# Performance work log

Measured on AMD Instinct MI355X. Metric: run time of the kernel, lower is better.

The kernel has to match this reference:

```python
import jax, jax.numpy as jnp
import numpy as np

B, N, C, L = 32, 1024, 128, 4

def setup_inputs() -> dict:
    key = jax.random.key(0)
    ks = jax.random.split(key, 8)
    x = jax.random.normal(ks[0], (B, N, C), dtype=jnp.float32)
    # binary adjacency: nonzero entries become unit-weight edges (edge weights unused in module)
    adj = jax.random.randint(ks[1], (B, N, N), 0, 2).astype(jnp.float32)
    mask = jnp.ones((B, N), dtype=jnp.float32)
    s = 1.0 / np.sqrt(C)
    weight = jax.random.uniform(ks[2], (L, C, C), minval=-s, maxval=s, dtype=jnp.float32)
    w_ih = jax.random.uniform(ks[3], (L, 3 * C, C), minval=-s, maxval=s, dtype=jnp.float32)
    w_hh = jax.random.uniform(ks[4], (L, 3 * C, C), minval=-s, maxval=s, dtype=jnp.float32)
    b_ih = jax.random.uniform(ks[5], (L, 3 * C), minval=-s, maxval=s, dtype=jnp.float32)
    b_hh = jax.random.uniform(ks[6], (L, 3 * C), minval=-s, maxval=s, dtype=jnp.float32)
    return {"x": x, "adj": adj, "mask": mask, "weight": weight,
            "w_ih": w_ih, "w_hh": w_hh, "b_ih": b_ih, "b_hh": b_hh}

def _gru_cell(m, h, w_ih, w_hh, b_ih, b_hh):
    # PyTorch GRUCell, gate order (r, z, n)
    gx = m @ w_ih.T + b_ih
    gh = h @ w_hh.T + b_hh
    xr, xz, xn = jnp.split(gx, 3, axis=-1)
    hr, hz, hn = jnp.split(gh, 3, axis=-1)
    r = jax.nn.sigmoid(xr + hr)
    z = jax.nn.sigmoid(xz + hz)
    n = jnp.tanh(xn + r * hn)
    return (1.0 - z) * n + z * h

def reference(x, adj, mask, weight, w_ih, w_hh, b_ih, b_hh):
    h = x  # [B, N, C]; in_channels == out_channels so no zero-padding needed
    for i in range(L):
        hw = jnp.einsum('bnc,cd->bnd', h, weight[i])
        # scatter-add of messages source->target == A^T @ (h W), unit edge weights
        m = jnp.einsum('bjn,bjd->bnd', adj, hw)
        h = _gru_cell(m, h, w_ih[i], w_hh[i], b_ih[i], b_hh[i])
    return h * mask[:, :, None]
```

## Files before the change

### kernel.cpp

```cpp
#include <hip/hip_runtime.h>
#include <stdint.h>


#define NB 32
#define NN 1024
#define NC 128
#define NL 4
#define MTOT (NB * NN)

#define MP 136

typedef __attribute__((ext_vector_type(8))) short s16x8;
typedef __attribute__((ext_vector_type(4))) float f32x4;
typedef __attribute__((ext_vector_type(2))) unsigned int u32x2;
typedef unsigned short U16;
typedef unsigned int U32;

__device__ __forceinline__ U16 f2bf(float f) {
    union { float f; U32 u; } v; v.f = f;
    return (U16)((v.u + 0x7FFFu + ((v.u >> 16) & 1u)) >> 16);
}
__device__ __forceinline__ float bf2f(U16 h) {
    union { U32 u; float f; } v; v.u = ((U32)h) << 16;
    return v.f;
}
__device__ __forceinline__ void splitbf(float x, U16& hi, U16& lo) {
    hi = f2bf(x);
    lo = f2bf(x - bf2f(hi));
}
__device__ __forceinline__ float sigmoidf_(float x) { return 1.f / (1.f + __expf(-x)); }

__device__ __forceinline__ void glds16(const void* g, void* l) {
    __builtin_amdgcn_global_load_lds(
        (const __attribute__((address_space(1))) void*)g,
        (__attribute__((address_space(3))) void*)l, 16, 0, 0);
}

#define SWZ(row, g) ((row) * 64 + ((((g) ^ ((row) & 7))) * 8))

__global__ __launch_bounds__(256) void k_setup(
    const float* __restrict__ adj, U16* __restrict__ adjT,
    const float* __restrict__ w, const float* __restrict__ wih, const float* __restrict__ whh,
    U16* __restrict__ wThi, U16* __restrict__ wTlo,
    U16* __restrict__ wihhi, U16* __restrict__ wihlo,
    U16* __restrict__ whhhi, U16* __restrict__ whhlo,
    const float* __restrict__ x, U16* __restrict__ hhi, U16* __restrict__ hlo)
{
    __shared__ float t[64 * 65];
    const int bid = blockIdx.x, tid = threadIdx.x;
    if (bid < 8192) {
        const int b = bid >> 8, rem = bid & 255;
        const int j0 = (rem & 15) * 64, n0 = (rem >> 4) * 64;
        const int rr = tid >> 4, c4 = (tid & 15) * 4;
#pragma unroll
        for (int p = 0; p < 4; ++p) {
            int j = p * 16 + rr;
            f32x4 v = *(const f32x4*)&adj[((size_t)b << 20) + ((size_t)(j0 + j) << 10) + n0 + c4];
#pragma unroll
            for (int u = 0; u < 4; ++u) t[j * 65 + c4 + u] = v[u];
        }
        __syncthreads();
#pragma unroll
        for (int p = 0; p < 4; ++p) {
            int n = p * 16 + rr;
            U16 h0 = f2bf(t[(c4 + 0) * 65 + n]);
            U16 h1 = f2bf(t[(c4 + 1) * 65 + n]);
            U16 h2 = f2bf(t[(c4 + 2) * 65 + n]);
            U16 h3 = f2bf(t[(c4 + 3) * 65 + n]);
            u32x2 pk; pk[0] = (U32)h0 | ((U32)h1 << 16); pk[1] = (U32)h2 | ((U32)h3 << 16);
            *(u32x2*)&adjT[((size_t)b << 20) + ((size_t)(n0 + n) << 10) + j0 + c4] = pk;
        }
    } else if (bid < 9984) {
        int i = (bid - 8192) * 256 + tid;
        if (i < 65536) {
            int l = i >> 14, rem = i & 16383, c = rem >> 7, d = rem & 127;
            U16 hi, lo; splitbf(w[i], hi, lo);
            int o = (l << 14) + (d << 7) + c;
            wThi[o] = hi; wTlo[o] = lo;
        } else if (i < 262144) {
            int j = i - 65536;
            U16 hi, lo; splitbf(wih[j], hi, lo);
            wihhi[j] = hi; wihlo[j] = lo;
        } else {
            int j = i - 262144;
            U16 hi, lo; splitbf(whh[j], hi, lo);
            whhhi[j] = hi; whhlo[j] = lo;
        }
    } else {
        int base = (bid - 9984) * 2048 + tid;
#pragma unroll
        for (int p = 0; p < 8; ++p) {
            int i = base + p * 256;
            U16 hi, lo; splitbf(x[i], hi, lo);
            hhi[i] = hi; hlo[i] = lo;
        }
    }
}

__global__ __launch_bounds__(256, 4) void k_hw2(
    const U16* __restrict__ Ahi, const U16* __restrict__ Alo,
    const U16* __restrict__ Bhi, const U16* __restrict__ Blo,
    U16* __restrict__ Ohi, U16* __restrict__ Olo)
{
    __shared__ union {
        struct { U16 Bh[128 * 64]; U16 Bl[128 * 64]; } bs;
        float bounce[64 * 129];
    } u;
    const int tid = threadIdx.x;
    const int lane = tid & 63, wv = tid >> 6;
    const int wd0 = wv * 32;
    const int lm = lane & 15, lk8 = (lane >> 4) * 8, quad = lane >> 4;
    const int m0 = blockIdx.x * 64;

    f32x4 acc[4][2] = {};

    for (int kc = 0; kc < 128; kc += 64) {
#pragma unroll
        for (int t = 0; t < 4; ++t) {
            int li = tid + t * 256; int d = li >> 3, sg = li & 7;
            int go = d * 128 + kc + ((sg ^ (d & 7)) * 8);
            glds16(&Bhi[go], &u.bs.Bh[li * 8]);
            glds16(&Blo[go], &u.bs.Bl[li * 8]);
        }
        __syncthreads();
#pragma unroll
        for (int ks = 0; ks < 2; ++ks) {
            const int k0 = kc + ks * 32 + lk8;
            const int g = ks * 4 + quad;
            s16x8 ahi[4], alo[4], bhi[2], blo[2];
#pragma unroll
            for (int q = 0; q < 4; ++q) {
                size_t ao = (size_t)(m0 + q * 16 + lm) * 128 + k0;
                ahi[q] = *(const s16x8*)&Ahi[ao];
                alo[q] = *(const s16x8*)&Alo[ao];
            }
#pragma unroll
            for (int q = 0; q < 2; ++q) {
                bhi[q] = *(const s16x8*)&u.bs.Bh[SWZ(wd0 + q * 16 + lm, g)];
                blo[q] = *(const s16x8*)&u.bs.Bl[SWZ(wd0 + q * 16 + lm, g)];
            }
#pragma unroll
            for (int rt = 0; rt < 4; ++rt)
#pragma unroll
                for (int ct = 0; ct < 2; ++ct) {
                    f32x4 a = acc[rt][ct];
                    a = __builtin_amdgcn_mfma_f32_16x16x32_bf16(ahi[rt], bhi[ct], a, 0, 0, 0);
                    a = __builtin_amdgcn_mfma_f32_16x16x32_bf16(ahi[rt], blo[ct], a, 0, 0, 0);
                    a = __builtin_amdgcn_mfma_f32_16x16x32_bf16(alo[rt], bhi[ct], a, 0, 0, 0);
                    acc[rt][ct] = a;
                }
        }
        __syncthreads();
    }

#pragma unroll
    for (int rt = 0; rt < 4; ++rt)
#pragma unroll
        for (int ct = 0; ct < 2; ++ct)
#pragma unroll
            for (int r = 0; r < 4; ++r)
                u.bounce[(rt * 16 + quad * 4 + r) * 129 + wd0 + ct * 16 + lm] = acc[rt][ct][r];
    __syncthreads();
    const int b = m0 >> 10, j0 = m0 & 1023;
#pragma unroll
    for (int t = 0; t < 16; ++t) {
        int i = tid + t * 256; int d = i >> 5, j2 = (i & 31) * 2;
        float x0 = u.bounce[j2 * 129 + d], x1 = u.bounce[(j2 + 1) * 129 + d];
        U16 h0, l0, h1, l1; splitbf(x0, h0, l0); splitbf(x1, h1, l1);
        size_t o = (((size_t)(b * 128 + d)) << 10) + j0 + j2;
        *(U32*)&Ohi[o] = (U32)h0 | ((U32)h1 << 16);
        *(U32*)&Olo[o] = (U32)l0 | ((U32)l1 << 16);
    }
}

__global__ __launch_bounds__(256, 2) void k_mega6(
    const U16* __restrict__ adjT,
    const U16* __restrict__ hwThi, const U16* __restrict__ hwTlo,
    const U16* __restrict__ hhi, const U16* __restrict__ hlo,
    const U16* __restrict__ wihhi, const U16* __restrict__ wihlo,
    const U16* __restrict__ whhhi, const U16* __restrict__ whhlo,
    const float* __restrict__ bih, const float* __restrict__ bhh,
    const float* __restrict__ mask,
    U16* __restrict__ houthi, U16* __restrict__ houtlo,
    float* __restrict__ out, int last)
{
    __shared__ union {
        struct { U16 As[2][64 * 64]; U16 Bh[2][128 * 64]; U16 Bl[2][128 * 64]; } st;
        struct { U16 Mhi[64 * MP]; U16 Mlo[64 * MP]; } m;
    } u;
    const int tid = threadIdx.x;
    const int lane = tid & 63, wv = tid >> 6;
    const int wd0 = wv * 32;
    const int lm = lane & 15, lk8 = (lane >> 4) * 8, quad = lane >> 4;
    const int xcd = blockIdx.x & 7;
    const int j = blockIdx.x >> 3;
    const int bt = xcd * 4 + (j >> 4);
    const int n0 = (j & 15) * 64;
    const int row0 = bt * NN + n0;

#define STAGE(kc, b)                                                                     \
    {                                                                                    \
        _Pragma("unroll")                                                                \
        for (int t = 0; t < 2; ++t) {                                                    \
            int li = tid + t * 256; int r = li >> 3, sg = li & 7;                        \
            glds16(&adjT[((size_t)bt << 20) + ((size_t)(n0 + r) << 10) + (kc)            \
                         + ((sg ^ (r & 7)) * 8)],                                        \
                   &u.st.As[b][li * 8]);                                                 \
        }                                                                                \
        _Pragma("unroll")                                                                \
        for (int t = 0; t < 4; ++t) {                                                    \
            int li = tid + t * 256; int d = li >> 3, sg = li & 7;                        \
            size_t o = (((size_t)(bt * 128 + d)) << 10) + (kc) + ((sg ^ (d & 7)) * 8);   \
            glds16(&hwThi[o], &u.st.Bh[b][li * 8]);                                      \
            glds16(&hwTlo[o], &u.st.Bl[b][li * 8]);                                      \
        }                                                                                \
    }

    f32x4 macc[4][2] = {};
    STAGE(0, 0);
    for (int c = 0; c < 16; ++c) {
        const int b = c & 1;
        __syncthreads();
        if (c + 1 < 16) STAGE((c + 1) * 64, b ^ 1);
#pragma unroll
        for (int ks = 0; ks < 2; ++ks) {
            const int g = ks * 4 + quad;
            s16x8 a[4], bh[2], bl[2];
#pragma unroll
            for (int q = 0; q < 4; ++q)
                a[q] = *(const s16x8*)&u.st.As[b][SWZ(q * 16 + lm, g)];
#pragma unroll
            for (int q = 0; q < 2; ++q) {
                bh[q] = *(const s16x8*)&u.st.Bh[b][SWZ(wd0 + q * 16 + lm, g)];
                bl[q] = *(const s16x8*)&u.st.Bl[b][SWZ(wd0 + q * 16 + lm, g)];
            }
#pragma unroll
            for (int rt = 0; rt < 4; ++rt)
#pragma unroll
                for (int ct = 0; ct < 2; ++ct) {
                    f32x4 cc = macc[rt][ct];
                    cc = __builtin_amdgcn_mfma_f32_16x16x32_bf16(a[rt], bh[ct], cc, 0, 0, 0);
                    cc = __builtin_amdgcn_mfma_f32_16x16x32_bf16(a[rt], bl[ct], cc, 0, 0, 0);
                    macc[rt][ct] = cc;
                }
        }
    }
#undef STAGE
    __syncthreads();

#pragma unroll
    for (int rt = 0; rt < 4; ++rt)
#pragma unroll
        for (int ct = 0; ct < 2; ++ct)
#pragma unroll
            for (int rr = 0; rr < 4; ++rr) {
                int rloc = rt * 16 + quad * 4 + rr;
                int d = wd0 + ct * 16 + lm;
                U16 hi, lo; splitbf(macc[rt][ct][rr], hi, lo);
                u.m.Mhi[rloc * MP + d] = hi;
                u.m.Mlo[rloc * MP + d] = lo;
            }

    f32x4 aR[4][2], aZ[4][2], aXN[4][2], aHN[4][2];
#pragma unroll
    for (int ct = 0; ct < 2; ++ct) {
        const int col = wd0 + ct * 16 + lm;
        const float bR  = bih[col]       + bhh[col];
        const float bZ  = bih[128 + col] + bhh[128 + col];
        const float bXN = bih[256 + col];
        const float bHN = bhh[256 + col];
#pragma unroll
        for (int rt = 0; rt < 4; ++rt) {
            aR[rt][ct]  = f32x4{bR, bR, bR, bR};
            aZ[rt][ct]  = f32x4{bZ, bZ, bZ, bZ};
            aXN[rt][ct] = f32x4{bXN, bXN, bXN, bXN};
            aHN[rt][ct] = f32x4{bHN, bHN, bHN, bHN};
        }
    }

    for (int cc = 0; cc < 4; ++cc) {
        const int ch = (cc + 2) & 3;
        if (cc == 2) __syncthreads();
        const U16* __restrict__ Whi = (ch < 2) ? wihhi : whhhi;
        const U16* __restrict__ Wlo = (ch < 2) ? wihlo : whhlo;
        const int kb = (ch & 1) * 64;
#pragma unroll
        for (int ks = 0; ks < 2; ++ks) {
            const int ko = kb + ks * 32 + lk8;
            s16x8 ahi[4], alo[4];
            if (ch < 2) {
#pragma unroll
                for (int q = 0; q < 4; ++q) {
                    ahi[q] = *(const s16x8*)&u.m.Mhi[(q * 16 + lm) * MP + ko];
                    alo[q] = *(const s16x8*)&u.m.Mlo[(q * 16 + lm) * MP + ko];
                }
            } else {
#pragma unroll
                for (int q = 0; q < 4; ++q) {
                    size_t ao = (size_t)(row0 + q * 16 + lm) * 128 + ko;
                    ahi[q] = *(const s16x8*)&hhi[ao];
                    alo[q] = *(const s16x8*)&hlo[ao];
                }
            }
#pragma unroll
            for (int ct = 0; ct < 2; ++ct) {
                const int col = wd0 + ct * 16 + lm;
                s16x8 bhiR = *(const s16x8*)&Whi[(size_t)col * 128 + ko];
                s16x8 bloR = *(const s16x8*)&Wlo[(size_t)col * 128 + ko];
                s16x8 bhiZ = *(const s16x8*)&Whi[(size_t)(128 + col) * 128 + ko];
                s16x8 bloZ = *(const s16x8*)&Wlo[(size_t)(128 + col) * 128 + ko];
                s16x8 bhiN = *(const s16x8*)&Whi[(size_t)(256 + col) * 128 + ko];
                s16x8 bloN = *(const s16x8*)&Wlo[(size_t)(256 + col) * 128 + ko];
#pragma unroll
                for (int rt = 0; rt < 4; ++rt) {
                    f32x4 r = aR[rt][ct];
                    r = __builtin_amdgcn_mfma_f32_16x16x32_bf16(ahi[rt], bhiR, r, 0, 0, 0);
                    r = __builtin_amdgcn_mfma_f32_16x16x32_bf16(ahi[rt], bloR, r, 0, 0, 0);
                    r = __builtin_amdgcn_mfma_f32_16x16x32_bf16(alo[rt], bhiR, r, 0, 0, 0);
                    aR[rt][ct] = r;
                    f32x4 z = aZ[rt][ct];
                    z = __builtin_amdgcn_mfma_f32_16x16x32_bf16(ahi[rt], bhiZ, z, 0, 0, 0);
                    z = __builtin_amdgcn_mfma_f32_16x16x32_bf16(ahi[rt], bloZ, z, 0, 0, 0);
                    z = __builtin_amdgcn_mfma_f32_16x16x32_bf16(alo[rt], bhiZ, z, 0, 0, 0);
                    aZ[rt][ct] = z;
                }
                if (ch < 2) {
#pragma unroll
                    for (int rt = 0; rt < 4; ++rt) {
                        f32x4 n = aXN[rt][ct];
                        n = __builtin_amdgcn_mfma_f32_16x16x32_bf16(ahi[rt], bhiN, n, 0, 0, 0);
                        n = __builtin_amdgcn_mfma_f32_16x16x32_bf16(ahi[rt], bloN, n, 0, 0, 0);
                        n = __builtin_amdgcn_mfma_f32_16x16x32_bf16(alo[rt], bhiN, n, 0, 0, 0);
                        aXN[rt][ct] = n;
                    }
                } else {
#pragma unroll
                    for (int rt = 0; rt < 4; ++rt) {
                        f32x4 n = aHN[rt][ct];
                        n = __builtin_amdgcn_mfma_f32_16x16x32_bf16(ahi[rt], bhiN, n, 0, 0, 0);
                        n = __builtin_amdgcn_mfma_f32_16x16x32_bf16(ahi[rt], bloN, n, 0, 0, 0);
                        n = __builtin_amdgcn_mfma_f32_16x16x32_bf16(alo[rt], bhiN, n, 0, 0, 0);
                        aHN[rt][ct] = n;
                    }
                }
            }
        }
    }

#pragma unroll
    for (int rt = 0; rt < 4; ++rt) {
#pragma unroll
        for (int ct = 0; ct < 2; ++ct) {
            const int col = wd0 + ct * 16 + lm;
#pragma unroll
            for (int rr = 0; rr < 4; ++rr) {
                const int row = row0 + rt * 16 + quad * 4 + rr;
                float r = sigmoidf_(aR[rt][ct][rr]);
                float z = sigmoidf_(aZ[rt][ct][rr]);
                float n = tanhf(aXN[rt][ct][rr] + r * aHN[rt][ct][rr]);
                size_t ho = (size_t)row * 128 + col;
                float hv = bf2f(hhi[ho]) + bf2f(hlo[ho]);
                float hnew = (1.f - z) * n + z * hv;
                if (last) {
                    out[ho] = hnew * mask[row];
                } else {
                    U16 hi2, lo2; splitbf(hnew, hi2, lo2);
                    houthi[ho] = hi2;
                    houtlo[ho] = lo2;
                }
            }
        }
    }
}

extern "C" void kernel_launch(void* const* d_in, const int* in_sizes, int n_in,
                              void* d_out, int out_size, void* d_ws, size_t ws_size,
                              hipStream_t stream) {
    (void)in_sizes; (void)n_in; (void)out_size; (void)ws_size;
    const float* x    = (const float*)d_in[0];
    const float* adj  = (const float*)d_in[1];
    const float* mask = (const float*)d_in[2];
    const float* wgt  = (const float*)d_in[3];
    const float* wih  = (const float*)d_in[4];
    const float* whh  = (const float*)d_in[5];
    const float* bih  = (const float*)d_in[6];
    const float* bhh  = (const float*)d_in[7];
    float* out = (float*)d_out;

    char* p = (char*)d_ws;
    U16* adjT    = (U16*)p;                p += (size_t)NB * NN * NN * 2;
    U16* h_hi    = (U16*)p;                p += (size_t)MTOT * NC * 2;
    U16* h_lo    = (U16*)p;                p += (size_t)MTOT * NC * 2;
    U16* hwT_hi  = (U16*)p;                p += (size_t)NB * NC * NN * 2;
    U16* hwT_lo  = (U16*)p;                p += (size_t)NB * NC * NN * 2;
    U16* wT_hi   = (U16*)p;                p += (size_t)NL * NC * NC * 2;
    U16* wT_lo   = (U16*)p;                p += (size_t)NL * NC * NC * 2;
    U16* wih_hi  = (U16*)p;                p += (size_t)NL * 384 * NC * 2;
    U16* wih_lo  = (U16*)p;                p += (size_t)NL * 384 * NC * 2;
    U16* whh_hi  = (U16*)p;                p += (size_t)NL * 384 * NC * 2;
    U16* whh_lo  = (U16*)p;                p += (size_t)NL * 384 * NC * 2;

    k_setup<<<12032, 256, 0, stream>>>(adj, adjT, wgt, wih, whh,
                                       wT_hi, wT_lo, wih_hi, wih_lo, whh_hi, whh_lo,
                                       x, h_hi, h_lo);

    for (int l = 0; l < NL; ++l) {
        k_hw2<<<512, 256, 0, stream>>>(h_hi, h_lo,
                                       wT_hi + l * 16384, wT_lo + l * 16384,
                                       hwT_hi, hwT_lo);
        k_mega6<<<512, 256, 0, stream>>>(adjT, hwT_hi, hwT_lo, h_hi, h_lo,
                                         wih_hi + l * 49152, wih_lo + l * 49152,
                                         whh_hi + l * 49152, whh_lo + l * 49152,
                                         bih + l * 384, bhh + l * 384, mask,
                                         h_hi, h_lo, out, (l == NL - 1) ? 1 : 0);
    }
}
```

Measured before the change: 519.7 us.

## Reassociate to (A^T h) W and fuse weight GEMM into mega kernel

Drops the separate h·W kernel by computing the aggregation A^T·h first and then multiplying by W inside the fused GRU kernel, using associativity. Each layer writes a transposed hi/lo copy of the new hidden state through an LDS bounce buffer, ping-ponged between two buffers, and setup produces the initial transposed x. This removes one launch per layer and the global write/read of hwT. In exchange the mega kernel does an extra in-LDS GEMM with weights read from global, and the rounding of the intermediate product changes.

```diff
diff --git a/kernel.cpp b/kernel.cpp
--- a/kernel.cpp
+++ b/kernel.cpp
@@ -44,7 +44,8 @@
     U16* __restrict__ wThi, U16* __restrict__ wTlo,
     U16* __restrict__ wihhi, U16* __restrict__ wihlo,
     U16* __restrict__ whhhi, U16* __restrict__ whhlo,
-    const float* __restrict__ x, U16* __restrict__ hhi, U16* __restrict__ hlo)
+    const float* __restrict__ x, U16* __restrict__ hhi, U16* __restrict__ hlo,
+    U16* __restrict__ hThi, U16* __restrict__ hTlo)
 {
     __shared__ float t[64 * 65];
     const int bid = blockIdx.x, tid = threadIdx.x;
@@ -70,8 +71,35 @@
             u32x2 pk; pk[0] = (U32)h0 | ((U32)h1 << 16); pk[1] = (U32)h2 | ((U32)h3 << 16);
             *(u32x2*)&adjT[((size_t)b << 20) + ((size_t)(n0 + n) << 10) + j0 + c4] = pk;
         }
-    } else if (bid < 9984) {
-        int i = (bid - 8192) * 256 + tid;
+    } else if (bid < 9216) {
+        const int bid2 = bid - 8192;
+        const int b = bid2 >> 5, rem = bid2 & 31;
+        const int j0 = (rem & 15) * 64, c0 = (rem >> 4) * 64;
+        const int rr = tid >> 4, c4 = (tid & 15) * 4;
+#pragma unroll
+        for (int p = 0; p < 4; ++p) {
+            int j = p * 16 + rr;
+            f32x4 v = *(const f32x4*)&x[(size_t)(b * 1024 + j0 + j) * 128 + c0 + c4];
+#pragma unroll
+            for (int u = 0; u < 4; ++u) t[j * 65 + c4 + u] = v[u];
+        }
+        __syncthreads();
+#pragma unroll
+        for (int p = 0; p < 4; ++p) {
+            int cl = p * 16 + rr;
+            U16 hi0, lo0, hi1, lo1, hi2, lo2, hi3, lo3;
+            splitbf(t[(c4 + 0) * 65 + cl], hi0, lo0);
+            splitbf(t[(c4 + 1) * 65 + cl], hi1, lo1);
+            splitbf(t[(c4 + 2) * 65 + cl], hi2, lo2);
+            splitbf(t[(c4 + 3) * 65 + cl], hi3, lo3);
+            size_t o = (((size_t)(b * 128 + c0 + cl)) << 10) + j0 + c4;
+            u32x2 ph; ph[0] = (U32)hi0 | ((U32)hi1 << 16); ph[1] = (U32)hi2 | ((U32)hi3 << 16);
+            u32x2 pl; pl[0] = (U32)lo0 | ((U32)lo1 << 16); pl[1] = (U32)lo2 | ((U32)lo3 << 16);
+            *(u32x2*)&hThi[o] = ph;
+            *(u32x2*)&hTlo[o] = pl;
+        }
+    } else if (bid < 11008) {
+        int i = (bid - 9216) * 256 + tid;
         if (i < 65536) {
             int l = i >> 14, rem = i & 16383, c = rem >> 7, d = rem & 127;
             U16 hi, lo; splitbf(w[i], hi, lo);
@@ -87,7 +115,7 @@
             whhhi[j] = hi; whhlo[j] = lo;
         }
     } else {
-        int base = (bid - 9984) * 2048 + tid;
+        int base = (bid - 11008) * 2048 + tid;
 #pragma unroll
         for (int p = 0; p < 8; ++p) {
             int i = base + p * 256;
@@ -97,96 +125,23 @@
     }
 }
 
-__global__ __launch_bounds__(256, 4) void k_hw2(
-    const U16* __restrict__ Ahi, const U16* __restrict__ Alo,
-    const U16* __restrict__ Bhi, const U16* __restrict__ Blo,
-    U16* __restrict__ Ohi, U16* __restrict__ Olo)
-{
-    __shared__ union {
-        struct { U16 Bh[128 * 64]; U16 Bl[128 * 64]; } bs;
-        float bounce[64 * 129];
-    } u;
-    const int tid = threadIdx.x;
-    const int lane = tid & 63, wv = tid >> 6;
-    const int wd0 = wv * 32;
-    const int lm = lane & 15, lk8 = (lane >> 4) * 8, quad = lane >> 4;
-    const int m0 = blockIdx.x * 64;
-
-    f32x4 acc[4][2] = {};
-
-    for (int kc = 0; kc < 128; kc += 64) {
-#pragma unroll
-        for (int t = 0; t < 4; ++t) {
-            int li = tid + t * 256; int d = li >> 3, sg = li & 7;
-            int go = d * 128 + kc + ((sg ^ (d & 7)) * 8);
-            glds16(&Bhi[go], &u.bs.Bh[li * 8]);
-            glds16(&Blo[go], &u.bs.Bl[li * 8]);
-        }
-        __syncthreads();
-#pragma unroll
-        for (int ks = 0; ks < 2; ++ks) {
-            const int k0 = kc + ks * 32 + lk8;
-            const int g = ks * 4 + quad;
-            s16x8 ahi[4], alo[4], bhi[2], blo[2];
-#pragma unroll
-            for (int q = 0; q < 4; ++q) {
-                size_t ao = (size_t)(m0 + q * 16 + lm) * 128 + k0;
-                ahi[q] = *(const s16x8*)&Ahi[ao];
-                alo[q] = *(const s16x8*)&Alo[ao];
-            }
-#pragma unroll
-            for (int q = 0; q < 2; ++q) {
-                bhi[q] = *(const s16x8*)&u.bs.Bh[SWZ(wd0 + q * 16 + lm, g)];
-                blo[q] = *(const s16x8*)&u.bs.Bl[SWZ(wd0 + q * 16 + lm, g)];
-            }
-#pragma unroll
-            for (int rt = 0; rt < 4; ++rt)
-#pragma unroll
-                for (int ct = 0; ct < 2; ++ct) {
-                    f32x4 a = acc[rt][ct];
-                    a = __builtin_amdgcn_mfma_f32_16x16x32_bf16(ahi[rt], bhi[ct], a, 0, 0, 0);
-                    a = __builtin_amdgcn_mfma_f32_16x16x32_bf16(ahi[rt], blo[ct], a, 0, 0, 0);
-                    a = __builtin_amdgcn_mfma_f32_16x16x32_bf16(alo[rt], bhi[ct], a, 0, 0, 0);
-                    acc[rt][ct] = a;
-                }
-        }
-        __syncthreads();
-    }
-
-#pragma unroll
-    for (int rt = 0; rt < 4; ++rt)
-#pragma unroll
-        for (int ct = 0; ct < 2; ++ct)
-#pragma unroll
-            for (int r = 0; r < 4; ++r)
-                u.bounce[(rt * 16 + quad * 4 + r) * 129 + wd0 + ct * 16 + lm] = acc[rt][ct][r];
-    __syncthreads();
-    const int b = m0 >> 10, j0 = m0 & 1023;
-#pragma unroll
-    for (int t = 0; t < 16; ++t) {
-        int i = tid + t * 256; int d = i >> 5, j2 = (i & 31) * 2;
-        float x0 = u.bounce[j2 * 129 + d], x1 = u.bounce[(j2 + 1) * 129 + d];
-        U16 h0, l0, h1, l1; splitbf(x0, h0, l0); splitbf(x1, h1, l1);
-        size_t o = (((size_t)(b * 128 + d)) << 10) + j0 + j2;
-        *(U32*)&Ohi[o] = (U32)h0 | ((U32)h1 << 16);
-        *(U32*)&Olo[o] = (U32)l0 | ((U32)l1 << 16);
-    }
-}
-
-__global__ __launch_bounds__(256, 2) void k_mega6(
+__global__ __launch_bounds__(256, 2) void k_mega8(
     const U16* __restrict__ adjT,
-    const U16* __restrict__ hwThi, const U16* __restrict__ hwTlo,
-    const U16* __restrict__ hhi, const U16* __restrict__ hlo,
+    const U16* __restrict__ hTinhi, const U16* __restrict__ hTinlo,
+    U16* __restrict__ hTouthi, U16* __restrict__ hToutlo,
+    U16* hhi, U16* hlo,
+    const U16* __restrict__ wtlhi, const U16* __restrict__ wtllo,
     const U16* __restrict__ wihhi, const U16* __restrict__ wihlo,
     const U16* __restrict__ whhhi, const U16* __restrict__ whhlo,
     const float* __restrict__ bih, const float* __restrict__ bhh,
     const float* __restrict__ mask,
-    U16* __restrict__ houthi, U16* __restrict__ houtlo,
     float* __restrict__ out, int last)
 {
     __shared__ union {
         struct { U16 As[2][64 * 64]; U16 Bh[2][128 * 64]; U16 Bl[2][128 * 64]; } st;
-        struct { U16 Mhi[64 * MP]; U16 Mlo[64 * MP]; } m;
+        struct { U16 Mhi[64 * MP]; U16 Mlo[64 * MP];
+                 char pad[40960 - 64 * MP * 4];
+                 float bounce[64 * 129]; } m;
     } u;
     const int tid = threadIdx.x;
     const int lane = tid & 63, wv = tid >> 6;
@@ -211,12 +166,12 @@
         for (int t = 0; t < 4; ++t) {                                                    \
             int li = tid + t * 256; int d = li >> 3, sg = li & 7;                        \
             size_t o = (((size_t)(bt * 128 + d)) << 10) + (kc) + ((sg ^ (d & 7)) * 8);   \
-            glds16(&hwThi[o], &u.st.Bh[b][li * 8]);                                      \
-            glds16(&hwTlo[o], &u.st.Bl[b][li * 8]);                                      \
+            glds16(&hTinhi[o], &u.st.Bh[b][li * 8]);                                     \
+            glds16(&hTinlo[o], &u.st.Bl[b][li * 8]);                                     \
         }                                                                                \
     }
 
-    f32x4 macc[4][2] = {};
+    f32x4 qacc[4][2] = {};
     STAGE(0, 0);
     for (int c = 0; c < 16; ++c) {
         const int b = c & 1;
@@ -238,14 +193,55 @@
             for (int rt = 0; rt < 4; ++rt)
 #pragma unroll
                 for (int ct = 0; ct < 2; ++ct) {
-                    f32x4 cc = macc[rt][ct];
+                    f32x4 cc = qacc[rt][ct];
                     cc = __builtin_amdgcn_mfma_f32_16x16x32_bf16(a[rt], bh[ct], cc, 0, 0, 0);
                     cc = __builtin_amdgcn_mfma_f32_16x16x32_bf16(a[rt], bl[ct], cc, 0, 0, 0);
-                    macc[rt][ct] = cc;
+                    qacc[rt][ct] = cc;
                 }
         }
     }
 #undef STAGE
+    __syncthreads();
+
+#pragma unroll
+    for (int rt = 0; rt < 4; ++rt)
+#pragma unroll
+        for (int ct = 0; ct < 2; ++ct)
+#pragma unroll
+            for (int rr = 0; rr < 4; ++rr) {
+                int rloc = rt * 16 + quad * 4 + rr;
+                int d = wd0 + ct * 16 + lm;
+                U16 hi, lo; splitbf(qacc[rt][ct][rr], hi, lo);
+                u.m.Mhi[rloc * MP + d] = hi;
+                u.m.Mlo[rloc * MP + d] = lo;
+            }
+    __syncthreads();
+
+    f32x4 macc[4][2] = {};
+#pragma unroll
+    for (int ks = 0; ks < 4; ++ks) {
+        const int ko = ks * 32 + lk8;
+        s16x8 qhi[4], qlo[4];
+#pragma unroll
+        for (int q = 0; q < 4; ++q) {
+            qhi[q] = *(const s16x8*)&u.m.Mhi[(q * 16 + lm) * MP + ko];
+            qlo[q] = *(const s16x8*)&u.m.Mlo[(q * 16 + lm) * MP + ko];
+        }
+#pragma unroll
+        for (int ct = 0; ct < 2; ++ct) {
+            const int col = wd0 + ct * 16 + lm;
+            s16x8 whi = *(const s16x8*)&wtlhi[col * 128 + ko];
+            s16x8 wlo = *(const s16x8*)&wtllo[col * 128 + ko];
+#pragma unroll
+            for (int rt = 0; rt < 4; ++rt) {
+                f32x4 cc = macc[rt][ct];
+                cc = __builtin_amdgcn_mfma_f32_16x16x32_bf16(qhi[rt], whi, cc, 0, 0, 0);
+                cc = __builtin_amdgcn_mfma_f32_16x16x32_bf16(qhi[rt], wlo, cc, 0, 0, 0);
+                cc = __builtin_amdgcn_mfma_f32_16x16x32_bf16(qlo[rt], whi, cc, 0, 0, 0);
+                macc[rt][ct] = cc;
+            }
+        }
+    }
     __syncthreads();
 
 #pragma unroll
@@ -354,7 +350,8 @@
             const int col = wd0 + ct * 16 + lm;
 #pragma unroll
             for (int rr = 0; rr < 4; ++rr) {
-                const int row = row0 + rt * 16 + quad * 4 + rr;
+                const int rloc = rt * 16 + quad * 4 + rr;
+                const int row = row0 + rloc;
                 float r = sigmoidf_(aR[rt][ct][rr]);
                 float z = sigmoidf_(aZ[rt][ct][rr]);
                 float n = tanhf(aXN[rt][ct][rr] + r * aHN[rt][ct][rr]);
@@ -365,10 +362,23 @@
                     out[ho] = hnew * mask[row];
                 } else {
                     U16 hi2, lo2; splitbf(hnew, hi2, lo2);
-                    houthi[ho] = hi2;
-                    houtlo[ho] = lo2;
-                }
-            }
+                    hhi[ho] = hi2;
+                    hlo[ho] = lo2;
+                    u.m.bounce[rloc * 129 + col] = hnew;
+                }
+            }
+        }
+    }
+    if (!last) {
+        __syncthreads();
+#pragma unroll
+        for (int t = 0; t < 16; ++t) {
+            int i = tid + t * 256; int c = i >> 5, j2 = (i & 31) * 2;
+            float x0 = u.m.bounce[j2 * 129 + c], x1 = u.m.bounce[(j2 + 1) * 129 + c];
+            U16 h0, l0, h1, l1; splitbf(x0, h0, l0); splitbf(x1, h1, l1);
+            size_t o = (((size_t)(bt * 128 + c)) << 10) + n0 + j2;
+            *(U32*)&hTouthi[o] = (U32)h0 | ((U32)h1 << 16);
+            *(U32*)&hToutlo[o] = (U32)l0 | ((U32)l1 << 16);
         }
     }
 }
@@ -391,8 +401,10 @@
     U16* adjT    = (U16*)p;                p += (size_t)NB * NN * NN * 2;
     U16* h_hi    = (U16*)p;                p += (size_t)MTOT * NC * 2;
     U16* h_lo    = (U16*)p;                p += (size_t)MTOT * NC * 2;
-    U16* hwT_hi  = (U16*)p;                p += (size_t)NB * NC * NN * 2;
-    U16* hwT_lo  = (U16*)p;                p += (size_t)NB * NC * NN * 2;
+    U16* hTa_hi  = (U16*)p;                p += (size_t)NB * NC * NN * 2;
+    U16* hTa_lo  = (U16*)p;                p += (size_t)NB * NC * NN * 2;
+    U16* hTb_hi  = (U16*)p;                p += (size_t)NB * NC * NN * 2;
+    U16* hTb_lo  = (U16*)p;                p += (size_t)NB * NC * NN * 2;
     U16* wT_hi   = (U16*)p;                p += (size_t)NL * NC * NC * 2;
     U16* wT_lo   = (U16*)p;                p += (size_t)NL * NC * NC * 2;
     U16* wih_hi  = (U16*)p;                p += (size_t)NL * 384 * NC * 2;
@@ -400,18 +412,21 @@
     U16* whh_hi  = (U16*)p;                p += (size_t)NL * 384 * NC * 2;
     U16* whh_lo  = (U16*)p;                p += (size_t)NL * 384 * NC * 2;
 
-    k_setup<<<12032, 256, 0, stream>>>(adj, adjT, wgt, wih, whh,
+    k_setup<<<13056, 256, 0, stream>>>(adj, adjT, wgt, wih, whh,
                                        wT_hi, wT_lo, wih_hi, wih_lo, whh_hi, whh_lo,
-                                       x, h_hi, h_lo);
+                                       x, h_hi, h_lo, hTa_hi, hTa_lo);
 
     for (int l = 0; l < NL; ++l) {
-        k_hw2<<<512, 256, 0, stream>>>(h_hi, h_lo,
-                                       wT_hi + l * 16384, wT_lo + l * 16384,
-                                       hwT_hi, hwT_lo);
-        k_mega6<<<512, 256, 0, stream>>>(adjT, hwT_hi, hwT_lo, h_hi, h_lo,
+        const U16* in_hi  = (l & 1) ? hTb_hi : hTa_hi;
+        const U16* in_lo  = (l & 1) ? hTb_lo : hTa_lo;
+        U16* out_hi       = (l & 1) ? hTa_hi : hTb_hi;
+        U16* out_lo       = (l & 1) ? hTa_lo : hTb_lo;
+        k_mega8<<<512, 256, 0, stream>>>(adjT, in_hi, in_lo, out_hi, out_lo,
+                                         h_hi, h_lo,
+                                         wT_hi + l * 16384, wT_lo + l * 16384,
                                          wih_hi + l * 49152, wih_lo + l * 49152,
                                          whh_hi + l * 49152, whh_lo + l * 49152,
                                          bih + l * 384, bhh + l * 384, mask,
-                                         h_hi, h_lo, out, (l == NL - 1) ? 1 : 0);
-    }
-}
+                                         out, (l == NL - 1) ? 1 : 0);
+    }
+}
```

Measured after the change: 576.3 us. 10.9% more time.
